# Performance work log

Measured on AMD Instinct MI355X. Metric: run time of the kernel, lower is better.

## Reference

```python
import jax, jax.numpy as jnp
import numpy as np

D, T, B, DEPTH, WIN, H = 1024, 2048, 4, 2, 128, 4
HD = D // H


def setup_inputs() -> dict:
    key = jax.random.key(0)
    ks = iter(jax.random.split(key, 32))
    s = D ** -0.5
    inp = {
        'x': jax.random.normal(next(ks), (B, T, D), jnp.float32),
        'ln1_s': jnp.ones((DEPTH, D)), 'ln1_b': jnp.zeros((DEPTH, D)),
        'ln2_s': jnp.ones((DEPTH, D)), 'ln2_b': jnp.zeros((DEPTH, D)),
        'ln3_s': jnp.ones((DEPTH, D)), 'ln3_b': jnp.zeros((DEPTH, D)),
        'rg_in_w': jax.random.normal(next(ks), (DEPTH, D, D)) * s,
        'rg_in_b': jnp.zeros((DEPTH, D)),
        'rg_gate_w': jax.random.normal(next(ks), (DEPTH, D, D)) * s,
        'rg_gate_b': jnp.zeros((DEPTH, D)),
        'rg_out_w': jax.random.normal(next(ks), (DEPTH, D, D)) * s,
        'rg_out_b': jnp.zeros((DEPTH, D)),
        'qkv_w': jax.random.normal(next(ks), (DEPTH, D, 3 * D)) * s,
        'qkv_b': jnp.zeros((DEPTH, 3 * D)),
        'attn_out_w': jax.random.normal(next(ks), (DEPTH, D, D)) * s,
        'attn_out_b': jnp.zeros((DEPTH, D)),
        'mlp_w1': jax.random.normal(next(ks), (DEPTH, D, 4 * D)) * s,
        'mlp_b1': jnp.zeros((DEPTH, 4 * D)),
        'mlp_w2': jax.random.normal(next(ks), (DEPTH, 4 * D, D)) * (4 * D) ** -0.5,
        'mlp_b2': jnp.zeros((DEPTH, D)),
    }
    return inp


def _ln(x, s, b):
    m = x.mean(-1, keepdims=True)
    v = ((x - m) ** 2).mean(-1, keepdims=True)
    return (x - m) / jnp.sqrt(v + 1e-5) * s + b


def _rg_lru(x, wi, bi, wg, bg, wo, bo):
    u = x @ wi + bi                      # [B,T,D]
    g = jax.nn.sigmoid(x @ wg + bg)      # [B,T,D]
    # h_t = g_t * h_{t-1} + (1-g_t) * u_t, h_{-1}=0 -> log-depth associative scan
    def comb(l, r):
        return (l[0] * r[0], r[0] * l[1] + r[1])
    _, h = jax.lax.associative_scan(comb, (g, (1.0 - g) * u), axis=1)
    return h @ wo + bo


def _local_attn(x, wqkv, bqkv, wo, bo):
    b, t, d = x.shape
    qkv = (x @ wqkv + bqkv).reshape(b, t, 3, H, HD)
    qkv = jnp.transpose(qkv, (2, 0, 3, 1, 4))  # [3,B,H,T,hd]
    q, k, v = qkv[0], qkv[1], qkv[2]
    scores = jnp.einsum('bhid,bhjd->bhij', q, k) / (HD ** 0.5)
    i = jnp.arange(t)[:, None]
    j = jnp.arange(t)[None, :]
    mask = (j <= i) & (j >= i - (WIN - 1))
    scores = jnp.where(mask, scores, -jnp.inf)
    p = jax.nn.softmax(scores, axis=-1)
    y = jnp.einsum('bhij,bhjd->bhid', p, v)
    y = jnp.transpose(y, (0, 2, 1, 3)).reshape(b, t, d)
    return y @ wo + bo


def reference(x, ln1_s, ln1_b, ln2_s, ln2_b, ln3_s, ln3_b,
              rg_in_w, rg_in_b, rg_gate_w, rg_gate_b, rg_out_w, rg_out_b,
              qkv_w, qkv_b, attn_out_w, attn_out_b,
              mlp_w1, mlp_b1, mlp_w2, mlp_b2):
    for l in range(DEPTH):
        x = x + _rg_lru(_ln(x, ln1_s[l], ln1_b[l]),
                        rg_in_w[l], rg_in_b[l], rg_gate_w[l], rg_gate_b[l],
                        rg_out_w[l], rg_out_b[l])
        x = x + _local_attn(_ln(x, ln2_s[l], ln2_b[l]),
                            qkv_w[l], qkv_b[l], attn_out_w[l], attn_out_b[l])
        h = _ln(x, ln3_s[l], ln3_b[l])
        h = jax.nn.gelu(h @ mlp_w1[l] + mlp_b1[l], approximate=False) @ mlp_w2[l] + mlp_b2[l]
        x = x + h
    return x
```

## Files before the change

### kernel.cpp

```cpp
#include <hip/hip_runtime.h>
#include <math.h>

#define DD 1024
#define TT 2048
#define BB 4
#define HH 4
#define HDIM 256
#define NLAYER 2
#define MM (BB*TT)
#define NCHUNK 32
#define CHUNK (TT/NCHUNK)

typedef unsigned short u16;
typedef __bf16 bf16x8 __attribute__((ext_vector_type(8)));
typedef float f32x4 __attribute__((ext_vector_type(4)));

__device__ __forceinline__ float b2f(u16 h) {
  unsigned u = ((unsigned)h) << 16;
  return __builtin_bit_cast(float, u);
}
__device__ __forceinline__ u16 f2b(float f) {
  unsigned u = __builtin_bit_cast(unsigned, f);
  u += 0x7fffu + ((u >> 16) & 1u);
  return (u16)(u >> 16);
}

#define GLD16(g, l) __builtin_amdgcn_global_load_lds( \
    (__attribute__((address_space(1))) void*)(void*)(g), \
    (__attribute__((address_space(3))) void*)(l), 16, 0, 0)

__device__ __forceinline__ void wg_barrier() {
  asm volatile("" ::: "memory");
  __builtin_amdgcn_s_barrier();
  asm volatile("" ::: "memory");
}
template<int N> __device__ __forceinline__ void wait_vmcnt() {
  asm volatile("s_waitcnt vmcnt(%0)" :: "i"(N) : "memory");
}

__global__ __launch_bounds__(256)
void transpose_cvt(const float* __restrict__ W, u16* __restrict__ Wt, int K, int N,
                   size_t lsrc, size_t ldst) {
  __shared__ float tile[32][33];
  const float* Wl = W + (size_t)blockIdx.z * lsrc;
  u16* Wtl = Wt + (size_t)blockIdx.z * ldst;
  const int n0 = blockIdx.x << 5, k0 = blockIdx.y << 5;
  const int tx = threadIdx.x, ty = threadIdx.y;
#pragma unroll
  for (int i = 0; i < 4; ++i)
    tile[ty + i*8][tx] = Wl[(size_t)(k0 + ty + i*8) * N + n0 + tx];
  __syncthreads();
#pragma unroll
  for (int i = 0; i < 4; ++i)
    Wtl[(size_t)(n0 + ty + i*8) * K + k0 + tx] = f2b(tile[tx][ty + i*8]);
}

__global__ __launch_bounds__(256)
void ln_k(const float* __restrict__ x, const float* __restrict__ sc,
          const float* __restrict__ bi, u16* __restrict__ xn) {
  const int row = blockIdx.x;
  const int tid = threadIdx.x;
  const float4 xv = ((const float4*)(x + (size_t)row * DD))[tid];
  float s = xv.x + xv.y + xv.z + xv.w;
  float q = xv.x*xv.x + xv.y*xv.y + xv.z*xv.z + xv.w*xv.w;
#pragma unroll
  for (int o = 1; o < 64; o <<= 1) { s += __shfl_xor(s, o); q += __shfl_xor(q, o); }
  __shared__ float rs[4], rq[4];
  if ((tid & 63) == 0) { rs[tid >> 6] = s; rq[tid >> 6] = q; }
  __syncthreads();
  s = rs[0] + rs[1] + rs[2] + rs[3];
  q = rq[0] + rq[1] + rq[2] + rq[3];
  const float mean = s * (1.f / DD);
  const float var = q * (1.f / DD) - mean * mean;
  const float rstd = rsqrtf(var + 1e-5f);
  const float4 sv = ((const float4*)sc)[tid];
  const float4 bv = ((const float4*)bi)[tid];
  const u16 o0 = f2b((xv.x - mean) * rstd * sv.x + bv.x);
  const u16 o1 = f2b((xv.y - mean) * rstd * sv.y + bv.y);
  const u16 o2 = f2b((xv.z - mean) * rstd * sv.z + bv.z);
  const u16 o3 = f2b((xv.w - mean) * rstd * sv.w + bv.w);
  uint2 pk;
  pk.x = (unsigned)o0 | ((unsigned)o1 << 16);
  pk.y = (unsigned)o2 | ((unsigned)o3 << 16);
  *(uint2*)(xn + (size_t)row * DD + (tid << 2)) = pk;
}

template<int EPI, int BN>
__global__ __launch_bounds__(512)
void gemm256t(const u16* __restrict__ A, const u16* __restrict__ Wt,
              const float* __restrict__ bias, const float* __restrict__ bias2,
              float* __restrict__ outf, u16* __restrict__ outb, int K, int N) {
  constexpr int NI = BN / 64;
  constexpr int PAIR = 2 + BN / 128;
  extern __shared__ u16 lds[];
  u16* Al = lds;
  u16* Bl = lds + 32768;
  const int tid = threadIdx.x;
  const int gx = gridDim.x;
  const int nwg = gx * (int)gridDim.y;
  int lid = (int)blockIdx.y * gx + (int)blockIdx.x;
  lid = (lid & 7) * (nwg >> 3) + (lid >> 3);
  const int m0 = (lid / gx) << 8;
  const int n0 = (lid % gx) * BN;
  const int lane = tid & 63;
  const int wid = tid >> 6;
  const int wm = wid >> 2;
  const int wn = wid & 3;
  const int g = lane >> 4;
  const int lc = lane & 15;
  const int rkey = (lc >> 1) & 3;
  const int q = tid >> 2;
  const int sslot = tid & 3;
  const int skey = (q >> 1) & 3;
  const int scs = (sslot ^ skey) << 3;
  const int so = (g ^ rkey) << 3;

  auto stage_pairP = [&](int p) {
    const int kt = p >> 1, buf = kt & 1, ch = p & 1;
    const int kbase = (kt << 6) + (ch << 5);
#pragma unroll
    for (int i = 0; i < 2; ++i) {
      const int row = i*128 + q;
      GLD16(A + (size_t)(m0 + row) * K + kbase + scs,
            Al + buf*16384 + ch*8192 + i*4096 + tid*8);
    }
#pragma unroll
    for (int i = 0; i < BN/128; ++i) {
      const int row = i*128 + q;
      GLD16(Wt + (size_t)(n0 + row) * K + kbase + scs,
            Bl + buf*(BN*64) + ch*(BN*32) + i*4096 + tid*8);
    }
  };
  auto read_set = [&](int p, bf16x8* af, bf16x8* bf) {
    const u16* Ab = Al + ((p >> 1) & 1)*16384 + (p & 1)*8192;
    const u16* Bb = Bl + ((p >> 1) & 1)*(BN*64) + (p & 1)*(BN*32);
#pragma unroll
    for (int ni = 0; ni < NI; ++ni)
      bf[ni] = *(const bf16x8*)(Bb + (wn*(NI*16) + ni*16 + lc)*32 + so);
#pragma unroll
    for (int i = 0; i < 4; ++i)
      af[i] = *(const bf16x8*)(Ab + (wm*128 + i*16 + lc)*32 + so);
#pragma unroll
    for (int i = 0; i < 4; ++i)
      af[4 + i] = *(const bf16x8*)(Ab + (wm*128 + 64 + i*16 + lc)*32 + so);
  };

  f32x4 acc[8][NI];
#pragma unroll
  for (int i = 0; i < 8; ++i)
#pragma unroll
    for (int j = 0; j < NI; ++j)
#pragma unroll
      for (int e = 0; e < 4; ++e) acc[i][j][e] = 0.f;

  const int KT = K >> 6;
  const int NP = KT << 1;
  stage_pairP(0); stage_pairP(1); stage_pairP(2);
  wait_vmcnt<2*PAIR>();
  wg_barrier();
  bf16x8 afX[8], bfX[NI], afY[8], bfY[NI];
  read_set(0, afX, bfX);

#define GPHASE(PP, CURA, CURB, NXTA, NXTB)                                          \
  {                                                                                 \
    const int P_ = (PP);                                                            \
    if (P_ + 1 < NP) {                                                              \
      if (P_ + 2 < NP) wait_vmcnt<PAIR>(); else wait_vmcnt<0>();                    \
      wg_barrier();                                                                 \
      read_set(P_ + 1, NXTA, NXTB);                                                 \
      if (P_ + 3 < NP) stage_pairP(P_ + 3);                                         \
    }                                                                               \
    __builtin_amdgcn_s_setprio(1);                                                  \
    _Pragma("unroll")                                                               \
    for (int i = 0; i < 8; ++i)                                                     \
      _Pragma("unroll")                                                             \
      for (int ni = 0; ni < NI; ++ni)                                               \
        acc[i][ni] = __builtin_amdgcn_mfma_f32_16x16x32_bf16(CURA[i], CURB[ni],     \
                                                             acc[i][ni], 0, 0, 0); \
    __builtin_amdgcn_s_setprio(0);                                                  \
  }

  for (int P = 0; P < NP; P += 2) {
    GPHASE(P,     afX, bfX, afY, bfY)
    GPHASE(P + 1, afY, bfY, afX, bfX)
  }
#undef GPHASE

#pragma unroll
  for (int mi = 0; mi < 8; ++mi) {
#pragma unroll
    for (int ni = 0; ni < NI; ++ni) {
      const int n = n0 + wn*(NI*16) + ni*16 + lc;
      const int mbase = m0 + wm*128 + (mi & 3)*16 + (mi >> 2)*64 + (g << 2);
      if (EPI == 4) {
        const float bia = bias[n];
        if (n < 2048) {
#pragma unroll
          for (int e = 0; e < 4; ++e)
            outb[(size_t)(mbase + e) * 2048 + n] = f2b(acc[mi][ni][e] + bia);
        } else {
          const int hh = (n - 2048) >> 8, dim = (n - 2048) & 255;
          const int bidx = mbase >> 11, t = mbase & 2047;
          const u16 a0 = f2b(acc[mi][ni][0] + bia);
          const u16 a1 = f2b(acc[mi][ni][1] + bia);
          const u16 a2 = f2b(acc[mi][ni][2] + bia);
          const u16 a3 = f2b(acc[mi][ni][3] + bia);
          uint2 pk;
          pk.x = (unsigned)a0 | ((unsigned)a1 << 16);
          pk.y = (unsigned)a2 | ((unsigned)a3 << 16);
          u16* vtp = (u16*)outf;
          *(uint2*)(vtp + ((size_t)((bidx*4 + hh)*256 + dim)) * 2048 + t) = pk;
        }
      } else if (EPI == 5) {
        const float bia = (n < 1024) ? bias[n] : bias2[n - 1024];
        u16* dst = (n < 1024) ? outb : (u16*)outf;
        const int nn = n & 1023;
#pragma unroll
        for (int e = 0; e < 4; ++e)
          dst[(size_t)(mbase + e) * 1024 + nn] = f2b(acc[mi][ni][e] + bia);
      } else if (EPI == 2) {
        const float bia = bias[n];
#pragma unroll
        for (int e = 0; e < 4; ++e) {
          const float v = acc[mi][ni][e] + bia;
          const float zc = fminf(fmaxf(1.5957691216f * (v + 0.044715f*v*v*v), -30.f), 30.f);
          outb[(size_t)(mbase + e) * N + n] = f2b(v / (1.f + __expf(-zc)));
        }
      } else {
        const float bia = bias[n];
#pragma unroll
        for (int e = 0; e < 4; ++e)
          outf[(size_t)(mbase + e) * N + n] += acc[mi][ni][e] + bia;
      }
    }
  }
}

__global__ __launch_bounds__(256)
void scan1_k(const u16* __restrict__ zpre, const u16* __restrict__ u,
             float* __restrict__ aggA, float* __restrict__ aggB) {
  const int d = blockIdx.x * 256 + threadIdx.x;
  const int c = blockIdx.y, b = blockIdx.z;
  const size_t base = ((size_t)b * TT + (size_t)c * CHUNK) * DD + d;
  float a = 1.f, acc = 0.f;
  for (int t = 0; t < CHUNK; ++t) {
    const float gl = 1.f / (1.f + __expf(-b2f(zpre[base + (size_t)t * DD])));
    const float ul = b2f(u[base + (size_t)t * DD]);
    acc = gl * acc + (1.f - gl) * ul;
    a *= gl;
  }
  const size_t o = ((size_t)b * NCHUNK + c) * DD + d;
  aggA[o] = a; aggB[o] = acc;
}

__global__ __launch_bounds__(256)
void scan2_k(const float* __restrict__ aggA, const float* __restrict__ aggB,
             float* __restrict__ carry) {
  const int idx = blockIdx.x * 256 + threadIdx.x;
  const int b = idx >> 10, d = idx & 1023;
  float h = 0.f;
  for (int c = 0; c < NCHUNK; ++c) {
    const size_t o = ((size_t)b * NCHUNK + c) * DD + d;
    carry[o] = h;
    h = aggA[o] * h + aggB[o];
  }
}

__global__ __launch_bounds__(256)
void scan3_k(const u16* __restrict__ zpre, const u16* __restrict__ u,
             const float* __restrict__ carry, u16* __restrict__ hout) {
  const int d = blockIdx.x * 256 + threadIdx.x;
  const int c = blockIdx.y, b = blockIdx.z;
  const size_t base = ((size_t)b * TT + (size_t)c * CHUNK) * DD + d;
  float h = carry[((size_t)b * NCHUNK + c) * DD + d];
  for (int t = 0; t < CHUNK; ++t) {
    const float gl = 1.f / (1.f + __expf(-b2f(zpre[base + (size_t)t * DD])));
    const float ul = b2f(u[base + (size_t)t * DD]);
    h = gl * h + (1.f - gl) * ul;
    hout[base + (size_t)t * DD] = f2b(h);
  }
}

__global__ __launch_bounds__(256)
void attn_mfma(const u16* __restrict__ qkb, const u16* __restrict__ vt,
               u16* __restrict__ y) {
  __shared__ u16 kv[16384];
  __shared__ u16 pb[4][16][200];
  const int tid = threadIdx.x;
  const int lane = tid & 63;
  const int wid = tid >> 6;
  const int g = lane >> 4;
  const int lc = lane & 15;
  const int t0 = blockIdx.x << 6;
  const int bh = blockIdx.y;
  const int bT = (bh >> 2) * TT;
  const int h = bh & 3;

  bf16x8 afq[8];
  {
    const u16* qg = qkb + (size_t)(bT + t0 + wid*16 + lc) * 2048 + h*256 + g*8;
#pragma unroll
    for (int ks = 0; ks < 8; ++ks)
      afq[ks] = __builtin_bit_cast(bf16x8, *(const uint4*)(qg + ks*32));
  }

  f32x4 sc[12];
#pragma unroll
  for (int f = 0; f < 12; ++f)
#pragma unroll
    for (int e = 0; e < 4; ++e) sc[f][e] = 0.f;

  const int koff = 1024 + h*256;
#pragma unroll
  for (int c = 0; c < 3; ++c) {
    const int j0 = t0 + (c - 2) * 64;
    if (j0 < 0) {
#pragma unroll
      for (int nt = 0; nt < 4; ++nt)
#pragma unroll
        for (int e = 0; e < 4; ++e) sc[c*4+nt][e] = -1e30f;
      continue;
    }
    __syncthreads();
    {
      const u16* kg = qkb + (size_t)(bT + j0) * 2048 + koff;
#pragma unroll
      for (int i = 0; i < 8; ++i) {
        const int o16 = i*256 + tid;
        const int slab = o16 >> 8, key = (o16 >> 2) & 63, ds = o16 & 3;
        GLD16(kg + (size_t)key*2048 + slab*32 + ds*8, kv + o16*8);
      }
    }
    __syncthreads();
#pragma unroll
    for (int nt = 0; nt < 4; ++nt) {
      f32x4 s = sc[c*4+nt];
#pragma unroll
      for (int ks = 0; ks < 8; ++ks) {
        const bf16x8 kb = *(const bf16x8*)(kv + ks*2048 + (nt*16 + lc)*32 + g*8);
        s = __builtin_amdgcn_mfma_f32_16x16x32_bf16(afq[ks], kb, s, 0, 0, 0);
      }
      sc[c*4+nt] = s;
    }
#pragma unroll
    for (int nt = 0; nt < 4; ++nt)
#pragma unroll
      for (int e = 0; e < 4; ++e) {
        const int tl = wid*16 + g*4 + e;
        const int jl = nt*16 + lc;
        const bool ok = (c == 1) || (c == 2 ? (jl <= tl) : (jl >= tl + 1));
        sc[c*4+nt][e] = ok ? sc[c*4+nt][e] * 0.0625f : -1e30f;
      }
  }

#pragma unroll
  for (int e = 0; e < 4; ++e) {
    float m = -1e30f;
#pragma unroll
    for (int f = 0; f < 12; ++f) m = fmaxf(m, sc[f][e]);
    m = fmaxf(m, __shfl_xor(m, 1)); m = fmaxf(m, __shfl_xor(m, 2));
    m = fmaxf(m, __shfl_xor(m, 4)); m = fmaxf(m, __shfl_xor(m, 8));
    float s = 0.f;
#pragma unroll
    for (int f = 0; f < 12; ++f) { const float p = __expf(sc[f][e] - m); sc[f][e] = p; s += p; }
    s += __shfl_xor(s, 1); s += __shfl_xor(s, 2);
    s += __shfl_xor(s, 4); s += __shfl_xor(s, 8);
    const float is = 1.f / s;
#pragma unroll
    for (int f = 0; f < 12; ++f) sc[f][e] *= is;
  }
#pragma unroll
  for (int c = 0; c < 3; ++c)
#pragma unroll
    for (int nt = 0; nt < 4; ++nt)
#pragma unroll
      for (int e = 0; e < 4; ++e)
        pb[wid][g*4 + e][c*64 + nt*16 + lc] = f2b(sc[c*4+nt][e]);

  f32x4 acc[16];
#pragma unroll
  for (int nt = 0; nt < 16; ++nt)
#pragma unroll
    for (int e = 0; e < 4; ++e) acc[nt][e] = 0.f;

  const u16* vg = vt + (size_t)bh * 256 * 2048;
#pragma unroll
  for (int c = 0; c < 3; ++c) {
    const int j0 = t0 + (c - 2) * 64;
    if (j0 < 0) continue;
    __syncthreads();
#pragma unroll
    for (int i = 0; i < 8; ++i) {
      const int o16 = i*256 + tid;
      const int dim = o16 >> 3, slot = o16 & 7;
      const int ss = slot ^ (dim & 7);
      GLD16(vg + (size_t)dim*2048 + j0 + ss*8, kv + o16*8);
    }
    __syncthreads();
#pragma unroll
    for (int ks = 0; ks < 2; ++ks) {
      const bf16x8 pa = *(const bf16x8*)&pb[wid][lc][(c*2 + ks)*32 + g*8];
#pragma unroll
      for (int nt = 0; nt < 16; ++nt) {
        const int dim = nt*16 + lc;
        int boff = dim*128 + ks*64 + g*16;
        boff ^= (dim & 7) << 4;
        const bf16x8 vb = *(const bf16x8*)((const char*)kv + boff);
        acc[nt] = __builtin_amdgcn_mfma_f32_16x16x32_bf16(pa, vb, acc[nt], 0, 0, 0);
      }
    }
  }

#pragma unroll
  for (int nt = 0; nt < 16; ++nt)
#pragma unroll
    for (int e = 0; e < 4; ++e) {
      const int tok = bT + t0 + wid*16 + g*4 + e;
      y[(size_t)tok * 1024 + h*256 + nt*16 + lc] = f2b(acc[nt][e]);
    }
}

extern "C" void kernel_launch(void* const* d_in, const int* in_sizes, int n_in,
                              void* d_out, int out_size, void* d_ws, size_t ws_size,
                              hipStream_t stream) {
  const float* x_in      = (const float*)d_in[0];
  const float* ln1_s     = (const float*)d_in[1];
  const float* ln1_b     = (const float*)d_in[2];
  const float* ln2_s     = (const float*)d_in[3];
  const float* ln2_b     = (const float*)d_in[4];
  const float* ln3_s     = (const float*)d_in[5];
  const float* ln3_b     = (const float*)d_in[6];
  const float* rg_in_w   = (const float*)d_in[7];
  const float* rg_in_b   = (const float*)d_in[8];
  const float* rg_gate_w = (const float*)d_in[9];
  const float* rg_gate_b = (const float*)d_in[10];
  const float* rg_out_w  = (const float*)d_in[11];
  const float* rg_out_b  = (const float*)d_in[12];
  const float* qkv_w     = (const float*)d_in[13];
  const float* qkv_b     = (const float*)d_in[14];
  const float* attn_out_w= (const float*)d_in[15];
  const float* attn_out_b= (const float*)d_in[16];
  const float* mlp_w1    = (const float*)d_in[17];
  const float* mlp_b1    = (const float*)d_in[18];
  const float* mlp_w2    = (const float*)d_in[19];
  const float* mlp_b2    = (const float*)d_in[20];

  hipFuncSetAttribute((const void*)&gemm256t<5,256>, hipFuncAttributeMaxDynamicSharedMemorySize, 131072);
  hipFuncSetAttribute((const void*)&gemm256t<4,256>, hipFuncAttributeMaxDynamicSharedMemorySize, 131072);
  hipFuncSetAttribute((const void*)&gemm256t<2,256>, hipFuncAttributeMaxDynamicSharedMemorySize, 131072);
  hipFuncSetAttribute((const void*)&gemm256t<3,128>, hipFuncAttributeMaxDynamicSharedMemorySize, 98304);

  float* x = (float*)d_out;
  char* ws = (char*)d_ws;
  u16*  wt     = (u16*)ws;
  u16*  xn     = (u16*)(ws + 62914560);
  char* bigS   = ws + 62914560 + 16777216;
  char* smallS = bigS + 67108864;
  float* aggA  = (float*)(smallS + 16777216);
  float* aggB  = aggA + (size_t)BB * NCHUNK * DD;
  float* carry = aggB + (size_t)BB * NCHUNK * DD;

  u16* ubuf = (u16*)bigS;
  u16* zbuf = (u16*)(bigS + 33554432);
  u16* qkb  = (u16*)bigS;
  u16* vtb  = (u16*)(bigS + 33554432);
  u16* hid  = (u16*)bigS;
  u16* hbuf = (u16*)smallS;
  u16* ybuf = (u16*)smallS;

  hipMemcpyAsync(x, x_in, (size_t)MM * DD * sizeof(float), hipMemcpyDeviceToDevice, stream);

  const size_t LW = 15728640;
  const dim3 tb(32, 8);
  transpose_cvt<<<dim3(32, 32, 2),  tb, 0, stream>>>(rg_in_w,    wt + 0,        DD, DD,   DD*DD,   LW);
  transpose_cvt<<<dim3(32, 32, 2),  tb, 0, stream>>>(rg_gate_w,  wt + 1048576,  DD, DD,   DD*DD,   LW);
  transpose_cvt<<<dim3(32, 32, 2),  tb, 0, stream>>>(rg_out_w,   wt + 2097152,  DD, DD,   DD*DD,   LW);
  transpose_cvt<<<dim3(96, 32, 2),  tb, 0, stream>>>(qkv_w,      wt + 3145728,  DD, 3072, DD*3072, LW);
  transpose_cvt<<<dim3(32, 32, 2),  tb, 0, stream>>>(attn_out_w, wt + 6291456,  DD, DD,   DD*DD,   LW);
  transpose_cvt<<<dim3(128, 32, 2), tb, 0, stream>>>(mlp_w1,     wt + 7340032,  DD, 4096, DD*4096, LW);
  transpose_cvt<<<dim3(32, 128, 2), tb, 0, stream>>>(mlp_w2,     wt + 11534336, 4096, DD, 4096*DD, LW);

  for (int l = 0; l < NLAYER; ++l) {
    u16* base = wt + (size_t)l * LW;
    ln_k<<<MM, 256, 0, stream>>>(x, ln1_s + l*DD, ln1_b + l*DD, xn);
    gemm256t<5,256><<<dim3(8, 32), 512, 131072, stream>>>(xn, base + 0, rg_in_b + l*DD, rg_gate_b + l*DD,
                                                          (float*)zbuf, ubuf, DD, 2048);
    scan1_k<<<dim3(4, NCHUNK, BB), 256, 0, stream>>>(zbuf, ubuf, aggA, aggB);
    scan2_k<<<16, 256, 0, stream>>>(aggA, aggB, carry);
    scan3_k<<<dim3(4, NCHUNK, BB), 256, 0, stream>>>(zbuf, ubuf, carry, hbuf);
    gemm256t<3,128><<<dim3(8, 32), 512, 98304, stream>>>(hbuf, base + 2097152, rg_out_b + l*DD, nullptr,
                                                         x, nullptr, DD, 1024);
    ln_k<<<MM, 256, 0, stream>>>(x, ln2_s + l*DD, ln2_b + l*DD, xn);
    gemm256t<4,256><<<dim3(12, 32), 512, 131072, stream>>>(xn, base + 3145728, qkv_b + l*3072, nullptr,
                                                           (float*)vtb, qkb, DD, 3072);
    attn_mfma<<<dim3(TT/64, BB*HH), 256, 0, stream>>>(qkb, vtb, ybuf);
    gemm256t<3,128><<<dim3(8, 32), 512, 98304, stream>>>(ybuf, base + 6291456, attn_out_b + l*DD, nullptr,
                                                         x, nullptr, DD, 1024);
    ln_k<<<MM, 256, 0, stream>>>(x, ln3_s + l*DD, ln3_b + l*DD, xn);
    gemm256t<2,256><<<dim3(16, 32), 512, 131072, stream>>>(xn, base + 7340032, mlp_b1 + l*4096, nullptr,
                                                           nullptr, hid, DD, 4096);
    gemm256t<3,128><<<dim3(8, 32), 512, 98304, stream>>>(hid, base + 11534336, mlp_b2 + l*DD, nullptr,
                                                         x, nullptr, 4096, 1024);
  }
}
```

Before: 900.5 us.

## Simplify GEMM to fixed 256x128 tiles with triple-buffered 32-wide K stages

Replaces the templated BN GEMM with a single 256x128 tile kernel. It uses a three-buffer LDS ring of 32-wide K slices, loaded with simple prefetch-two-ahead staging, in place of the paired-phase double-buffered register pipeline. LDS use drops to 72KB and the launch bound requests more occupancy, while grids for the wider-N GEMMs double. The trade is one barrier per 32 K instead of per 32 with register double-buffering, less A-tile reuse across N for the wide GEMMs, and less overlap of LDS reads with MFMA.

```diff
diff --git a/kernel.cpp b/kernel.cpp
--- a/kernel.cpp
+++ b/kernel.cpp
@@ -85,113 +85,83 @@
   *(uint2*)(xn + (size_t)row * DD + (tid << 2)) = pk;
 }
 
-template<int EPI, int BN>
-__global__ __launch_bounds__(512)
+template<int EPI>
+__global__ __launch_bounds__(512, 4)
 void gemm256t(const u16* __restrict__ A, const u16* __restrict__ Wt,
               const float* __restrict__ bias, const float* __restrict__ bias2,
               float* __restrict__ outf, u16* __restrict__ outb, int K, int N) {
-  constexpr int NI = BN / 64;
-  constexpr int PAIR = 2 + BN / 128;
   extern __shared__ u16 lds[];
-  u16* Al = lds;
-  u16* Bl = lds + 32768;
   const int tid = threadIdx.x;
   const int gx = gridDim.x;
   const int nwg = gx * (int)gridDim.y;
   int lid = (int)blockIdx.y * gx + (int)blockIdx.x;
   lid = (lid & 7) * (nwg >> 3) + (lid >> 3);
   const int m0 = (lid / gx) << 8;
-  const int n0 = (lid % gx) * BN;
+  const int n0 = (lid % gx) << 7;
   const int lane = tid & 63;
   const int wid = tid >> 6;
   const int wm = wid >> 2;
   const int wn = wid & 3;
   const int g = lane >> 4;
   const int lc = lane & 15;
-  const int rkey = (lc >> 1) & 3;
   const int q = tid >> 2;
-  const int sslot = tid & 3;
-  const int skey = (q >> 1) & 3;
-  const int scs = (sslot ^ skey) << 3;
-  const int so = (g ^ rkey) << 3;
-
-  auto stage_pairP = [&](int p) {
-    const int kt = p >> 1, buf = kt & 1, ch = p & 1;
-    const int kbase = (kt << 6) + (ch << 5);
-#pragma unroll
-    for (int i = 0; i < 2; ++i) {
-      const int row = i*128 + q;
-      GLD16(A + (size_t)(m0 + row) * K + kbase + scs,
-            Al + buf*16384 + ch*8192 + i*4096 + tid*8);
-    }
-#pragma unroll
-    for (int i = 0; i < BN/128; ++i) {
-      const int row = i*128 + q;
-      GLD16(Wt + (size_t)(n0 + row) * K + kbase + scs,
-            Bl + buf*(BN*64) + ch*(BN*32) + i*4096 + tid*8);
-    }
+  const int slot = tid & 3;
+  const int scs = (slot ^ ((q >> 1) & 3)) << 3;
+  const int so = (g ^ ((lc >> 1) & 3)) << 3;
+
+  u16* Ab = lds;
+  u16* Bbase = lds + 24576;
+  u16 *Ac = Ab, *An = Ab + 8192, *Aw = Ab + 16384;
+  u16 *Bc = Bbase, *Bn = Bbase + 4096, *Bw = Bbase + 8192;
+
+  auto stage = [&](int kt, u16* At, u16* Bt) {
+    const int kb = (kt << 5) + scs;
+    GLD16(A + (size_t)(m0 + q) * K + kb,       At + q*32 + slot*8);
+    GLD16(A + (size_t)(m0 + 128 + q) * K + kb, At + (128 + q)*32 + slot*8);
+    GLD16(Wt + (size_t)(n0 + q) * K + kb,      Bt + q*32 + slot*8);
   };
-  auto read_set = [&](int p, bf16x8* af, bf16x8* bf) {
-    const u16* Ab = Al + ((p >> 1) & 1)*16384 + (p & 1)*8192;
-    const u16* Bb = Bl + ((p >> 1) & 1)*(BN*64) + (p & 1)*(BN*32);
-#pragma unroll
-    for (int ni = 0; ni < NI; ++ni)
-      bf[ni] = *(const bf16x8*)(Bb + (wn*(NI*16) + ni*16 + lc)*32 + so);
-#pragma unroll
-    for (int i = 0; i < 4; ++i)
-      af[i] = *(const bf16x8*)(Ab + (wm*128 + i*16 + lc)*32 + so);
-#pragma unroll
-    for (int i = 0; i < 4; ++i)
-      af[4 + i] = *(const bf16x8*)(Ab + (wm*128 + 64 + i*16 + lc)*32 + so);
-  };
-
-  f32x4 acc[8][NI];
+
+  f32x4 acc[8][2];
 #pragma unroll
   for (int i = 0; i < 8; ++i)
 #pragma unroll
-    for (int j = 0; j < NI; ++j)
+    for (int j = 0; j < 2; ++j)
 #pragma unroll
       for (int e = 0; e < 4; ++e) acc[i][j][e] = 0.f;
 
-  const int KT = K >> 6;
-  const int NP = KT << 1;
-  stage_pairP(0); stage_pairP(1); stage_pairP(2);
-  wait_vmcnt<2*PAIR>();
-  wg_barrier();
-  bf16x8 afX[8], bfX[NI], afY[8], bfY[NI];
-  read_set(0, afX, bfX);
-
-#define GPHASE(PP, CURA, CURB, NXTA, NXTB)                                          \
-  {                                                                                 \
-    const int P_ = (PP);                                                            \
-    if (P_ + 1 < NP) {                                                              \
-      if (P_ + 2 < NP) wait_vmcnt<PAIR>(); else wait_vmcnt<0>();                    \
-      wg_barrier();                                                                 \
-      read_set(P_ + 1, NXTA, NXTB);                                                 \
-      if (P_ + 3 < NP) stage_pairP(P_ + 3);                                         \
-    }                                                                               \
-    __builtin_amdgcn_s_setprio(1);                                                  \
-    _Pragma("unroll")                                                               \
-    for (int i = 0; i < 8; ++i)                                                     \
-      _Pragma("unroll")                                                             \
-      for (int ni = 0; ni < NI; ++ni)                                               \
-        acc[i][ni] = __builtin_amdgcn_mfma_f32_16x16x32_bf16(CURA[i], CURB[ni],     \
-                                                             acc[i][ni], 0, 0, 0); \
-    __builtin_amdgcn_s_setprio(0);                                                  \
-  }
-
-  for (int P = 0; P < NP; P += 2) {
-    GPHASE(P,     afX, bfX, afY, bfY)
-    GPHASE(P + 1, afY, bfY, afX, bfX)
-  }
-#undef GPHASE
+  const int KT = K >> 5;
+  stage(0, Ac, Bc);
+  stage(1, An, Bn);
+
+  for (int kt = 0; kt < KT; ++kt) {
+    if (kt + 1 < KT) wait_vmcnt<3>();
+    else             wait_vmcnt<0>();
+    wg_barrier();
+    bf16x8 bf0 = *(const bf16x8*)(Bc + (wn*32 + lc)*32 + so);
+    bf16x8 bf1 = *(const bf16x8*)(Bc + (wn*32 + 16 + lc)*32 + so);
+    bf16x8 af[8];
+#pragma unroll
+    for (int i = 0; i < 8; ++i)
+      af[i] = *(const bf16x8*)(Ac + (wm*128 + i*16 + lc)*32 + so);
+    if (kt + 2 < KT) stage(kt + 2, Aw, Bw);
+    __builtin_amdgcn_s_setprio(1);
+#pragma unroll
+    for (int i = 0; i < 8; ++i) {
+      acc[i][0] = __builtin_amdgcn_mfma_f32_16x16x32_bf16(af[i], bf0, acc[i][0], 0, 0, 0);
+      acc[i][1] = __builtin_amdgcn_mfma_f32_16x16x32_bf16(af[i], bf1, acc[i][1], 0, 0, 0);
+    }
+    __builtin_amdgcn_s_setprio(0);
+    u16* t;
+    t = Ac; Ac = An; An = Aw; Aw = t;
+    t = Bc; Bc = Bn; Bn = Bw; Bw = t;
+  }
 
 #pragma unroll
   for (int mi = 0; mi < 8; ++mi) {
 #pragma unroll
-    for (int ni = 0; ni < NI; ++ni) {
-      const int n = n0 + wn*(NI*16) + ni*16 + lc;
-      const int mbase = m0 + wm*128 + (mi & 3)*16 + (mi >> 2)*64 + (g << 2);
+    for (int ni = 0; ni < 2; ++ni) {
+      const int n = n0 + wn*32 + ni*16 + lc;
+      const int mbase = m0 + wm*128 + mi*16 + (g << 2);
       if (EPI == 4) {
         const float bia = bias[n];
         if (n < 2048) {
@@ -445,10 +415,10 @@
   const float* mlp_w2    = (const float*)d_in[19];
   const float* mlp_b2    = (const float*)d_in[20];
 
-  hipFuncSetAttribute((const void*)&gemm256t<5,256>, hipFuncAttributeMaxDynamicSharedMemorySize, 131072);
-  hipFuncSetAttribute((const void*)&gemm256t<4,256>, hipFuncAttributeMaxDynamicSharedMemorySize, 131072);
-  hipFuncSetAttribute((const void*)&gemm256t<2,256>, hipFuncAttributeMaxDynamicSharedMemorySize, 131072);
-  hipFuncSetAttribute((const void*)&gemm256t<3,128>, hipFuncAttributeMaxDynamicSharedMemorySize, 98304);
+  hipFuncSetAttribute((const void*)&gemm256t<5>, hipFuncAttributeMaxDynamicSharedMemorySize, 73728);
+  hipFuncSetAttribute((const void*)&gemm256t<4>, hipFuncAttributeMaxDynamicSharedMemorySize, 73728);
+  hipFuncSetAttribute((const void*)&gemm256t<2>, hipFuncAttributeMaxDynamicSharedMemorySize, 73728);
+  hipFuncSetAttribute((const void*)&gemm256t<3>, hipFuncAttributeMaxDynamicSharedMemorySize, 73728);
 
   float* x = (float*)d_out;
   char* ws = (char*)d_ws;
@@ -483,23 +453,23 @@
   for (int l = 0; l < NLAYER; ++l) {
     u16* base = wt + (size_t)l * LW;
     ln_k<<<MM, 256, 0, stream>>>(x, ln1_s + l*DD, ln1_b + l*DD, xn);
-    gemm256t<5,256><<<dim3(8, 32), 512, 131072, stream>>>(xn, base + 0, rg_in_b + l*DD, rg_gate_b + l*DD,
-                                                          (float*)zbuf, ubuf, DD, 2048);
+    gemm256t<5><<<dim3(16, 32), 512, 73728, stream>>>(xn, base + 0, rg_in_b + l*DD, rg_gate_b + l*DD,
+                                                      (float*)zbuf, ubuf, DD, 2048);
     scan1_k<<<dim3(4, NCHUNK, BB), 256, 0, stream>>>(zbuf, ubuf, aggA, aggB);
     scan2_k<<<16, 256, 0, stream>>>(aggA, aggB, carry);
     scan3_k<<<dim3(4, NCHUNK, BB), 256, 0, stream>>>(zbuf, ubuf, carry, hbuf);
-    gemm256t<3,128><<<dim3(8, 32), 512, 98304, stream>>>(hbuf, base + 2097152, rg_out_b + l*DD, nullptr,
-                                                         x, nullptr, DD, 1024);
+    gemm256t<3><<<dim3(8, 32), 512, 73728, stream>>>(hbuf, base + 2097152, rg_out_b + l*DD, nullptr,
+                                                     x, nullptr, DD, 1024);
     ln_k<<<MM, 256, 0, stream>>>(x, ln2_s + l*DD, ln2_b + l*DD, xn);
-    gemm256t<4,256><<<dim3(12, 32), 512, 131072, stream>>>(xn, base + 3145728, qkv_b + l*3072, nullptr,
-                                                           (float*)vtb, qkb, DD, 3072);
+    gemm256t<4><<<dim3(24, 32), 512, 73728, stream>>>(xn, base + 3145728, qkv_b + l*3072, nullptr,
+                                                      (float*)vtb, qkb, DD, 3072);
     attn_mfma<<<dim3(TT/64, BB*HH), 256, 0, stream>>>(qkb, vtb, ybuf);
-    gemm256t<3,128><<<dim3(8, 32), 512, 98304, stream>>>(ybuf, base + 6291456, attn_out_b + l*DD, nullptr,
-                                                         x, nullptr, DD, 1024);
+    gemm256t<3><<<dim3(8, 32), 512, 73728, stream>>>(ybuf, base + 6291456, attn_out_b + l*DD, nullptr,
+                                                     x, nullptr, DD, 1024);
     ln_k<<<MM, 256, 0, stream>>>(x, ln3_s + l*DD, ln3_b + l*DD, xn);
-    gemm256t<2,256><<<dim3(16, 32), 512, 131072, stream>>>(xn, base + 7340032, mlp_b1 + l*4096, nullptr,
-                                                           nullptr, hid, DD, 4096);
-    gemm256t<3,128><<<dim3(8, 32), 512, 98304, stream>>>(hid, base + 11534336, mlp_b2 + l*DD, nullptr,
-                                                         x, nullptr, 4096, 1024);
-  }
-}
+    gemm256t<2><<<dim3(32, 32), 512, 73728, stream>>>(xn, base + 7340032, mlp_b1 + l*4096, nullptr,
+                                                      nullptr, hid, DD, 4096);
+    gemm256t<3><<<dim3(8, 32), 512, 73728, stream>>>(hid, base + 11534336, mlp_b2 + l*DD, nullptr,
+                                                     x, nullptr, 4096, 1024);
+  }
+}
```

Result: no change. 899.6 us (-0.1%).
